# Kernel optimization log

Measured on AMD Instinct MI355X. Metric: run time of the kernel, lower is better.

The kernel has to match this reference:

```python
import jax, jax.numpy as jnp
import numpy as np
import math

B, S = 2, 2048
DIM_MODEL = 2048
NUM_Q_HEADS = 16
GROUP_SIZE = 4
NUM_KV_HEADS = NUM_Q_HEADS // GROUP_SIZE
DIM_K = 128
RMS_EPS = 1e-6
ROPE_BASE = 10000.0


def setup_inputs() -> dict:
    key = jax.random.key(0)
    ks = jax.random.split(key, 8)
    x = jax.random.normal(ks[0], (B, S, DIM_MODEL), dtype=jnp.float32)
    mask = jnp.tril(jnp.ones((S, S), dtype=bool))  # causal
    # Linear weights stored as [in, out] so y = x @ W (bias=False everywhere)
    sd = 1.0 / math.sqrt(DIM_MODEL)
    Wq = jax.random.uniform(ks[1], (DIM_MODEL, DIM_K * NUM_Q_HEADS), jnp.float32, -sd, sd)
    Wk = jax.random.uniform(ks[2], (DIM_MODEL, DIM_K * NUM_KV_HEADS), jnp.float32, -sd, sd)
    Wv = jax.random.uniform(ks[3], (DIM_MODEL, DIM_K * NUM_KV_HEADS), jnp.float32, -sd, sd)
    sf = 1.0 / math.sqrt(DIM_K * NUM_Q_HEADS)
    Wfc = jax.random.uniform(ks[4], (DIM_K * NUM_Q_HEADS, DIM_MODEL), jnp.float32, -sf, sf)
    q_gamma = jnp.ones((DIM_K,), dtype=jnp.float32)
    k_gamma = jnp.ones((DIM_K,), dtype=jnp.float32)
    return {"x": x, "mask": mask, "Wq": Wq, "Wk": Wk, "Wv": Wv,
            "Wfc": Wfc, "q_gamma": q_gamma, "k_gamma": k_gamma}


def _rope(t):
    # t: [B, H, S, D], rotate-half RoPE
    d = t.shape[-1]
    half = d // 2
    inv_freq = 1.0 / (ROPE_BASE ** (jnp.arange(half, dtype=jnp.float32) / half))
    pos = jnp.arange(t.shape[2], dtype=jnp.float32)
    ang = pos[:, None] * inv_freq[None, :]            # [S, half]
    cos, sin = jnp.cos(ang), jnp.sin(ang)              # [S, half]
    t1, t2 = t[..., :half], t[..., half:]
    return jnp.concatenate([t1 * cos - t2 * sin, t2 * cos + t1 * sin], axis=-1)


def _rmsnorm(t, gamma):
    ms = jnp.mean(t * t, axis=-1, keepdims=True)
    return t * jax.lax.rsqrt(ms + RMS_EPS) * gamma


def reference(x, mask, Wq, Wk, Wv, Wfc, q_gamma, k_gamma):
    b, s, _ = x.shape
    q = (x @ Wq).reshape(b, s, NUM_Q_HEADS, DIM_K).transpose(0, 2, 1, 3)   # [B,Hq,S,D]
    k = (x @ Wk).reshape(b, s, NUM_KV_HEADS, DIM_K).transpose(0, 2, 1, 3)  # [B,Hkv,S,D]
    v = (x @ Wv).reshape(b, s, NUM_KV_HEADS, DIM_K).transpose(0, 2, 1, 3)
    q = _rmsnorm(_rope(q), q_gamma)
    k = _rmsnorm(_rope(k), k_gamma)
    q = q.reshape(b, NUM_KV_HEADS, GROUP_SIZE, s, DIM_K)                    # [B,Hkv,G,S,D]
    scores = jnp.einsum('bhgqd,bhkd->bhgqk', q, k) / math.sqrt(DIM_K)      # [B,Hkv,G,S,S]
    scores = jnp.where(mask, scores, -jnp.inf)
    attn = jax.nn.softmax(scores, axis=-1)  # dropout is identity in eval
    out = jnp.einsum('bhgqk,bhkd->bhgqd', attn, v)                          # [B,Hkv,G,S,D]
    out = out.reshape(b, NUM_Q_HEADS, s, DIM_K).transpose(0, 2, 1, 3)
    out = out.reshape(b, s, NUM_Q_HEADS * DIM_K) @ Wfc                      # [B,S,DM]
    return out
```

## Files before the change

kernel.cpp:

```cpp
#include <hip/hip_runtime.h>
#include <hip/hip_bf16.h>

typedef __attribute__((ext_vector_type(8))) short bf16x8;
typedef __attribute__((ext_vector_type(4))) short bf16x4;
typedef __attribute__((ext_vector_type(4))) float f32x4;

#define S_LEN 2048
#define DMODEL 2048
#define NQH 16
#define NKVH 4
#define DK 128

__device__ __forceinline__ float b2f(short u) {
  union { unsigned int i; float f; } x;
  x.i = ((unsigned int)(unsigned short)u) << 16;
  return x.f;
}
__device__ __forceinline__ short f2b(float f) {
  union { float f; unsigned int i; } x; x.f = f;
  unsigned int r = (x.i + 0x7fffu + ((x.i >> 16) & 1u)) >> 16;
  return (short)r;
}
__device__ __forceinline__ unsigned int cvtpk(float a, float b) {
  unsigned int r;
  asm("v_cvt_pk_bf16_f32 %0, %1, %2" : "=v"(r) : "v"(a), "v"(b));
  return r;
}
__device__ __forceinline__ f32x4 mfma16(bf16x8 a, bf16x8 b, f32x4 c) {
  return __builtin_amdgcn_mfma_f32_16x16x32_bf16(a, b, c, 0, 0, 0);
}
__device__ __forceinline__ void async16(short* lds, const short* g) {
  __builtin_amdgcn_global_load_lds(
      (const __attribute__((address_space(1))) unsigned int*)(const void*)g,
      (__attribute__((address_space(3))) unsigned int*)(void*)lds, 16, 0, 0);
}

__global__ void f32_to_bf16(const float* __restrict__ in, short* __restrict__ out, int n4) {
  int i = blockIdx.x * blockDim.x + threadIdx.x;
  if (i >= n4) return;
  float4 v = ((const float4*)in)[i];
  bf16x4 o;
  o[0] = f2b(v.x); o[1] = f2b(v.y); o[2] = f2b(v.z); o[3] = f2b(v.w);
  ((bf16x4*)out)[i] = o;
}

__device__ __forceinline__ void transpose_tile(const float* __restrict__ in,
                                               short* __restrict__ out, int R, int C,
                                               int bx, int by, int tid, short (*t)[33]) {
  const int c0 = bx * 32, r0 = by * 32;
  const int tx = tid & 31, ty = tid >> 5;
#pragma unroll
  for (int i = 0; i < 32; i += 8)
    t[ty + i][tx] = f2b(in[(size_t)(r0 + ty + i) * C + c0 + tx]);
  __syncthreads();
#pragma unroll
  for (int i = 0; i < 32; i += 8)
    out[(size_t)(c0 + ty + i) * R + r0 + tx] = t[tx][ty + i];
}

__global__ __launch_bounds__(256) void prep_kernel(const float* __restrict__ Wq,
                                                   const float* __restrict__ Wk,
                                                   const float* __restrict__ Wv,
                                                   const float* __restrict__ Wfc,
                                                   short* __restrict__ WqT,
                                                   short* __restrict__ WkT,
                                                   short* __restrict__ WvT,
                                                   short* __restrict__ WfcT,
                                                   float* __restrict__ rt) {
  __shared__ short t[32][33];
  const int id = blockIdx.x;
  const int tid = threadIdx.x;
  if (id < 4096) {
    transpose_tile(Wq, WqT, 2048, 2048, id & 63, id >> 6, tid, t);
  } else if (id < 5120) {
    const int r = id - 4096;
    transpose_tile(Wk, WkT, 2048, 512, r & 15, r >> 4, tid, t);
  } else if (id < 6144) {
    const int r = id - 5120;
    transpose_tile(Wv, WvT, 2048, 512, r & 15, r >> 4, tid, t);
  } else if (id < 10240) {
    const int r = id - 6144;
    transpose_tile(Wfc, WfcT, 2048, 2048, r & 63, r >> 6, tid, t);
  } else {
    const int i = (id - 10240) * 256 + tid;
    const int s = i >> 6, d = i & 63;
    float ang = (float)s * __expf((float)d * -0.14391157f);
    float c, sn;
    __sincosf(ang, &sn, &c);
    rt[s * 128 + d] = c;
    rt[s * 128 + 64 + d] = sn;
  }
}

__device__ __forceinline__ void stage_tile64(short* Ls, const short* Gb, int ldg,
                                             int w, int lane) {
#pragma unroll
  for (int i = 0; i < 4; ++i) {
    const int r0 = w * 32 + i * 8;
    const int row = r0 + (lane >> 3);
    const int colb = ((lane & 7) * 8) ^ ((row & 7) << 3);
    async16(Ls + r0 * 64, Gb + (size_t)row * ldg + colb);
  }
}

__global__ __launch_bounds__(256) void gemm_qkv(const short* __restrict__ A,
                                                const short* __restrict__ WT,
                                                short* __restrict__ Qr,
                                                short* __restrict__ Kr,
                                                short* __restrict__ Vtr,
                                                const float* __restrict__ qg,
                                                const float* __restrict__ kg,
                                                const float* __restrict__ ropeT) {
  constexpr int CS_LD = 136;
  __shared__ __align__(16) short smem[4 * 128 * 64];

  const int flat = blockIdx.x;
  const int xcd = flat & 7, idx = flat >> 3;
  const int mb = (xcd >> 1) * 8 + (idx & 7);
  const int nb = (xcd & 1) * 12 + (idx >> 3);

  const int tid = threadIdx.x;
  const int lane = tid & 63;
  const int w = tid >> 6;
  const int wm = w >> 1, wn = w & 1;
  const int l15 = lane & 15, lg = lane >> 4;
  const int K = DMODEL;
  constexpr int NSTEP = DMODEL / 64;

  f32x4 acc[4][4] = {};
  const short* Ab = A + (size_t)mb * 128 * K;
  const short* Bb = WT + (size_t)nb * 128 * K;

  stage_tile64(smem, Ab, K, w, lane);
  stage_tile64(smem + 8192, Bb, K, w, lane);
  asm volatile("s_waitcnt vmcnt(0)" ::: "memory");
  __syncthreads();

  for (int t = 0; t < NSTEP; ++t) {
    const int cur = t & 1;
    short* Ac = smem + cur * 16384;
    short* Bc = Ac + 8192;
    if (t + 1 < NSTEP) {
      short* An = smem + (cur ^ 1) * 16384;
      stage_tile64(An, Ab + (t + 1) * 64, K, w, lane);
      stage_tile64(An + 8192, Bb + (t + 1) * 64, K, w, lane);
    }
#pragma unroll
    for (int kk = 0; kk < 2; ++kk) {
      bf16x8 af[4], bfr[4];
#pragma unroll
      for (int mt = 0; mt < 4; ++mt)
        af[mt] = *(const bf16x8*)(Ac + (wm * 64 + mt * 16 + l15) * 64 +
                                  ((kk * 32 + lg * 8) ^ ((l15 & 7) << 3)));
#pragma unroll
      for (int nt = 0; nt < 4; ++nt)
        bfr[nt] = *(const bf16x8*)(Bc + (wn * 64 + nt * 16 + l15) * 64 +
                                   ((kk * 32 + lg * 8) ^ ((l15 & 7) << 3)));
#pragma unroll
      for (int mt = 0; mt < 4; ++mt)
#pragma unroll
        for (int nt = 0; nt < 4; ++nt)
          acc[mt][nt] = mfma16(af[mt], bfr[nt], acc[mt][nt]);
    }
    asm volatile("s_waitcnt vmcnt(0)" ::: "memory");
    __syncthreads();
  }

  short* Cs = smem;
#pragma unroll
  for (int mt = 0; mt < 4; ++mt)
#pragma unroll
    for (int nt = 0; nt < 4; ++nt)
#pragma unroll
      for (int r = 0; r < 4; ++r)
        Cs[(wm * 64 + mt * 16 + lg * 4 + r) * CS_LD + wn * 64 + nt * 16 + l15] =
            f2b(acc[mt][nt][r]);
  __syncthreads();

  const int srow0 = mb * 128;
  const int b = srow0 >> 11;

  if (nb < 20) {
    const bool isQ = nb < 16;
    const int h = isQ ? nb : nb - 16;
    const float* gamma = isQ ? qg : kg;
    const int r = tid >> 1, half = tid & 1;
    const int s = (srow0 + r) & 2047;
    const float* rt = ropeT + (size_t)s * 128;
    float ss = 0.f;
    bf16x8 ov[8];
#pragma unroll
    for (int j = 0; j < 8; ++j) {
      bf16x8 t1v = *(const bf16x8*)(Cs + r * CS_LD + j * 8);
      bf16x8 t2v = *(const bf16x8*)(Cs + r * CS_LD + 64 + j * 8);
      float4 c0 = *(const float4*)(rt + j * 8);
      float4 c1 = *(const float4*)(rt + j * 8 + 4);
      float4 s0 = *(const float4*)(rt + 64 + j * 8);
      float4 s1 = *(const float4*)(rt + 64 + j * 8 + 4);
      float cc[8] = {c0.x, c0.y, c0.z, c0.w, c1.x, c1.y, c1.z, c1.w};
      float sn[8] = {s0.x, s0.y, s0.z, s0.w, s1.x, s1.y, s1.z, s1.w};
#pragma unroll
      for (int i = 0; i < 8; ++i) {
        float t1 = b2f(t1v[i]), t2 = b2f(t2v[i]);
        float o = half ? (t2 * cc[i] + t1 * sn[i]) : (t1 * cc[i] - t2 * sn[i]);
        ss += o * o;
        ov[j][i] = f2b(o);
      }
    }
    ss += __shfl_xor(ss, 1);
    float inv = rsqrtf(ss * (1.0f / 128.0f) + 1e-6f);
    if (isQ) inv *= (0.08838834764831845f * 1.4426950408889634f);
    const int NH = isQ ? NQH : NKVH;
    short* outp = isQ ? Qr : Kr;
    short* ob = outp + ((size_t)(b * NH + h) * S_LEN + s) * DK + half * 64;
#pragma unroll
    for (int j = 0; j < 8; ++j) {
      float4 g0 = *(const float4*)(gamma + half * 64 + j * 8);
      float4 g1 = *(const float4*)(gamma + half * 64 + j * 8 + 4);
      float gg[8] = {g0.x, g0.y, g0.z, g0.w, g1.x, g1.y, g1.z, g1.w};
      bf16x8 vv;
#pragma unroll
      for (int i = 0; i < 8; ++i) vv[i] = f2b(b2f(ov[j][i]) * inv * gg[i]);
      *(bf16x8*)(ob + j * 8) = vv;
    }
  } else {
    const int h = nb - 20;
    const int d = tid & 127;
    const int sh = tid >> 7;
    const int sbase = (srow0 & 2047) + sh * 64;
    short* ob = Vtr + ((size_t)(b * NKVH + h) * DK + d) * S_LEN + sbase;
    for (int i0 = 0; i0 < 64; i0 += 8) {
      bf16x8 v;
#pragma unroll
      for (int j = 0; j < 8; ++j) {
        const int p = i0 + j;
        const int sl = sh * 64 + 16 * (p & 3) + (p >> 2);
        v[j] = Cs[sl * CS_LD + d];
      }
      *(bf16x8*)(ob + i0) = v;
    }
  }
}

__global__ __launch_bounds__(256) void gemm_out(const short* __restrict__ A,
                                                const short* __restrict__ BT,
                                                float* __restrict__ outf) {
  __shared__ __align__(16) short smem[4 * 128 * 64];

  const int flat = blockIdx.x;
  const int xcd = flat & 7, idx = flat >> 3;
  const int mb = (xcd >> 1) * 8 + (idx & 7);
  const int nb = (xcd & 1) * 8 + (idx >> 3);

  const int tid = threadIdx.x;
  const int lane = tid & 63;
  const int w = tid >> 6;
  const int wm = w >> 1, wn = w & 1;
  const int l15 = lane & 15, lg = lane >> 4;
  const int K = NQH * DK, N = DMODEL;
  constexpr int NSTEP = (NQH * DK) / 64;

  f32x4 acc[4][4] = {};
  const short* Ab = A + (size_t)mb * 128 * K;
  const short* Bb = BT + (size_t)nb * 128 * K;

  stage_tile64(smem, Ab, K, w, lane);
  stage_tile64(smem + 8192, Bb, K, w, lane);
  asm volatile("s_waitcnt vmcnt(0)" ::: "memory");
  __syncthreads();

  for (int t = 0; t < NSTEP; ++t) {
    const int cur = t & 1;
    short* Ac = smem + cur * 16384;
    short* Bc = Ac + 8192;
    if (t + 1 < NSTEP) {
      short* An = smem + (cur ^ 1) * 16384;
      stage_tile64(An, Ab + (t + 1) * 64, K, w, lane);
      stage_tile64(An + 8192, Bb + (t + 1) * 64, K, w, lane);
    }
#pragma unroll
    for (int kk = 0; kk < 2; ++kk) {
      bf16x8 af[4], bfr[4];
#pragma unroll
      for (int mt = 0; mt < 4; ++mt)
        af[mt] = *(const bf16x8*)(Ac + (wm * 64 + mt * 16 + l15) * 64 +
                                  ((kk * 32 + lg * 8) ^ ((l15 & 7) << 3)));
#pragma unroll
      for (int nt = 0; nt < 4; ++nt)
        bfr[nt] = *(const bf16x8*)(Bc + (wn * 64 + nt * 16 + l15) * 64 +
                                   ((kk * 32 + lg * 8) ^ ((l15 & 7) << 3)));
#pragma unroll
      for (int mt = 0; mt < 4; ++mt)
#pragma unroll
        for (int nt = 0; nt < 4; ++nt)
          acc[mt][nt] = mfma16(af[mt], bfr[nt], acc[mt][nt]);
    }
    asm volatile("s_waitcnt vmcnt(0)" ::: "memory");
    __syncthreads();
  }

#pragma unroll
  for (int mt = 0; mt < 4; ++mt) {
    const int row = mb * 128 + wm * 64 + mt * 16 + lg * 4;
#pragma unroll
    for (int nt = 0; nt < 4; ++nt) {
      const int col = nb * 128 + wn * 64 + nt * 16 + l15;
#pragma unroll
      for (int r = 0; r < 4; ++r)
        outf[(size_t)(row + r) * N + col] = acc[mt][nt][r];
    }
  }
}

__device__ __forceinline__ void stage_kv(const short* __restrict__ Kb,
                                         const short* __restrict__ Vb, int kb,
                                         short* Ks, short* Vs, int w, int lane) {
#pragma unroll
  for (int i = 0; i < 4; ++i) {
    const int c = 4 * w + i;
    const int krow = c * 4 + (lane >> 4);
    const int kcol = (((lane & 15) * 16) ^ ((krow & 7) << 4)) >> 1;
    async16(Ks + c * 512, Kb + (size_t)(kb + krow) * DK + kcol);
    const int vrow = c * 8 + (lane >> 3);
    const int vcol = (((lane & 7) * 16) ^ ((vrow & 7) << 4)) >> 1;
    async16(Vs + c * 512, Vb + (size_t)vrow * S_LEN + kb + vcol);
  }
}

__device__ __forceinline__ void sm_pv(f32x4* sc, float* lsum, f32x4* acco,
                                      const short* Vc, short* Pw, int q0, bool diag,
                                      int kb, int l15, int lg) {
  if (diag) {
#pragma unroll
    for (int nt = 0; nt < 4; ++nt) {
      const int k = kb + nt * 16 + l15;
#pragma unroll
      for (int r = 0; r < 4; ++r)
        if (k > q0 + lg * 4 + r) sc[nt][r] = -1e30f;
    }
  }
#pragma unroll
  for (int r = 0; r < 4; ++r) {
    const float p0 = exp2f(sc[0][r]);
    const float p1 = exp2f(sc[1][r]);
    const float p2 = exp2f(sc[2][r]);
    const float p3 = exp2f(sc[3][r]);
    lsum[r] += (p0 + p1) + (p2 + p3);
    uint2 dv;
    dv.x = cvtpk(p0, p1);
    dv.y = cvtpk(p2, p3);
    *(uint2*)(Pw + (lg * 4 + r) * 72 + l15 * 4) = dv;
  }
#pragma unroll
  for (int kk = 0; kk < 2; ++kk) {
    bf16x8 ap = *(const bf16x8*)(Pw + l15 * 72 + kk * 32 + lg * 8);
#pragma unroll
    for (int dt = 0; dt < 8; ++dt) {
      const int vrow = dt * 16 + l15;
      bf16x8 bv = *(const bf16x8*)(Vc + vrow * 64 +
                                   (((kk * 64 + lg * 16) ^ ((vrow & 7) << 4)) >> 1));
      acco[dt] = mfma16(ap, bv, acco[dt]);
    }
  }
}

__device__ __forceinline__ void attn_writeout(f32x4* acco, float* lsum,
                                              short* __restrict__ AO, int b, int qh,
                                              int q0, int l15, int lg) {
  float ls[4];
#pragma unroll
  for (int r = 0; r < 4; ++r) {
    float t = lsum[r];
    t += __shfl_xor(t, 1);
    t += __shfl_xor(t, 2);
    t += __shfl_xor(t, 4);
    t += __shfl_xor(t, 8);
    ls[r] = 1.0f / t;
  }
  short* ob = AO + (size_t)(b * S_LEN + q0) * (NQH * DK) + qh * DK;
#pragma unroll
  for (int dt = 0; dt < 8; ++dt)
#pragma unroll
    for (int r = 0; r < 4; ++r)
      ob[(size_t)(lg * 4 + r) * (NQH * DK) + dt * 16 + l15] = f2b(acco[dt][r] * ls[r]);
}

__global__ __launch_bounds__(256, 2) void attn_kernel(const short* __restrict__ Qr,
                                                      const short* __restrict__ Kr,
                                                      const short* __restrict__ Vt,
                                                      short* __restrict__ AO) {
  const int flat = blockIdx.x;
  const int nw = (flat & 7) * 64 + (flat >> 3);
  const int qtA = nw & 15;
  const int bh = nw >> 4;
  const int qtB = 31 - qtA;
  const int b = bh >> 4, qh = bh & 15;
  const int kvh = qh >> 2;
  const short* Qb = Qr + (size_t)bh * S_LEN * DK;
  const short* Kb = Kr + (size_t)(b * NKVH + kvh) * S_LEN * DK;
  const short* Vb = Vt + (size_t)(b * NKVH + kvh) * DK * S_LEN;
  const int tid = threadIdx.x, lane = tid & 63, w = tid >> 6;
  const int l15 = lane & 15, lg = lane >> 4;

  __shared__ __align__(16) short KV[4][64 * 128];
  __shared__ __align__(16) short P[4][16][72];
  short* Pw = &P[w][0][0];

  const int q0A = qtA * 64 + w * 16, q0B = qtB * 64 + w * 16;
  bf16x8 aqA[4], aqB[4];
#pragma unroll
  for (int kk = 0; kk < 4; ++kk) {
    aqA[kk] = *(const bf16x8*)(Qb + (size_t)(q0A + l15) * DK + kk * 32 + lg * 8);
    aqB[kk] = *(const bf16x8*)(Qb + (size_t)(q0B + l15) * DK + kk * 32 + lg * 8);
  }

  f32x4 accoA[8] = {}, accoB[8] = {};
  float lsA[4] = {0.f, 0.f, 0.f, 0.f}, lsB[4] = {0.f, 0.f, 0.f, 0.f};

  short* Kcur = KV[0]; short* Vcur = KV[1];
  short* Knxt = KV[2]; short* Vnxt = KV[3];

  stage_kv(Kb, Vb, 0, Kcur, Vcur, w, lane);
  asm volatile("s_waitcnt vmcnt(0)" ::: "memory");
  __syncthreads();

  for (int kt = 0; kt <= qtB; ++kt) {
    const int kb = kt * 64;
    if (kt < qtB) stage_kv(Kb, Vb, kb + 64, Knxt, Vnxt, w, lane);

    if (kt <= qtA) {
      f32x4 scB[4] = {}, scA[4] = {};
#pragma unroll
      for (int kk = 0; kk < 4; ++kk)
#pragma unroll
        for (int nt = 0; nt < 4; ++nt) {
          const int krow = nt * 16 + l15;
          bf16x8 bk = *(const bf16x8*)(Kcur + krow * 128 +
                                       (((kk * 64 + lg * 16) ^ ((krow & 7) << 4)) >> 1));
          scB[nt] = mfma16(aqB[kk], bk, scB[nt]);
          scA[nt] = mfma16(aqA[kk], bk, scA[nt]);
        }
      sm_pv(scB, lsB, accoB, Vcur, Pw, q0B, false, kb, l15, lg);
      sm_pv(scA, lsA, accoA, Vcur, Pw, q0A, kt == qtA, kb, l15, lg);
    } else {
      f32x4 scB[4] = {};
#pragma unroll
      for (int kk = 0; kk < 4; ++kk)
#pragma unroll
        for (int nt = 0; nt < 4; ++nt) {
          const int krow = nt * 16 + l15;
          bf16x8 bk = *(const bf16x8*)(Kcur + krow * 128 +
                                       (((kk * 64 + lg * 16) ^ ((krow & 7) << 4)) >> 1));
          scB[nt] = mfma16(aqB[kk], bk, scB[nt]);
        }
      sm_pv(scB, lsB, accoB, Vcur, Pw, q0B, kt == qtB, kb, l15, lg);
    }

    asm volatile("s_waitcnt vmcnt(0)" ::: "memory");
    __syncthreads();
    short* t;
    t = Kcur; Kcur = Knxt; Knxt = t;
    t = Vcur; Vcur = Vnxt; Vnxt = t;
  }

  attn_writeout(accoB, lsB, AO, b, qh, q0B, l15, lg);
  attn_writeout(accoA, lsA, AO, b, qh, q0A, l15, lg);
}

extern "C" void kernel_launch(void* const* d_in, const int* in_sizes, int n_in,
                              void* d_out, int out_size, void* d_ws, size_t ws_size,
                              hipStream_t stream) {
  const float* x = (const float*)d_in[0];
  const float* Wq = (const float*)d_in[2];
  const float* Wk = (const float*)d_in[3];
  const float* Wv = (const float*)d_in[4];
  const float* Wfc = (const float*)d_in[5];
  const float* qg = (const float*)d_in[6];
  const float* kg = (const float*)d_in[7];

  short* ws = (short*)d_ws;
  short* xb = ws;
  short* WqkvT = xb + (size_t)4096 * 2048;
  short* WqT = WqkvT;
  short* WkT = WqT + (size_t)2048 * 2048;
  short* WvT = WkT + (size_t)512 * 2048;
  short* WfcT = WvT + (size_t)512 * 2048;
  short* Qr = WfcT + (size_t)2048 * 2048;
  short* Kr = Qr + (size_t)32 * 2048 * 128;
  short* Vt = Kr + (size_t)8 * 2048 * 128;
  float* ropeT = (float*)(Vt + (size_t)8 * 128 * 2048);
  short* AO = xb;

  f32_to_bf16<<<(4096 * 2048 / 4 + 255) / 256, 256, 0, stream>>>(x, xb, 4096 * 2048 / 4);
  prep_kernel<<<10752, 256, 0, stream>>>(Wq, Wk, Wv, Wfc, WqT, WkT, WvT, WfcT, ropeT);

  gemm_qkv<<<768, 256, 0, stream>>>(xb, WqkvT, Qr, Kr, Vt, qg, kg, ropeT);

  attn_kernel<<<512, 256, 0, stream>>>(Qr, Kr, Vt, AO);

  gemm_out<<<512, 256, 0, stream>>>(AO, WfcT, (float*)d_out);
}
```

Measured before the change: 191.6 us.

## Shrink GEMM K-step to 32 for 4-block occupancy and fold x conversion into prep

The fp32-to-bf16 conversion of x moves into the prep kernel, removing one launch. The two GEMMs share a new core that stages 32-wide K slices with a different XOR swizzle, which cuts LDS from 64KB to 32KB and sets launch_bounds(256,4) so more blocks fit per CU. The QKV epilogue now processes the 128-row tile in two 64-row phases to fit the smaller LDS, with four threads per row for RoPE and RMSNorm. The cost is twice as many barriers per K and more serialized epilogue phases.

```diff
diff --git a/kernel.cpp b/kernel.cpp
--- a/kernel.cpp
+++ b/kernel.cpp
@@ -35,15 +35,6 @@
       (__attribute__((address_space(3))) unsigned int*)(void*)lds, 16, 0, 0);
 }
 
-__global__ void f32_to_bf16(const float* __restrict__ in, short* __restrict__ out, int n4) {
-  int i = blockIdx.x * blockDim.x + threadIdx.x;
-  if (i >= n4) return;
-  float4 v = ((const float4*)in)[i];
-  bf16x4 o;
-  o[0] = f2b(v.x); o[1] = f2b(v.y); o[2] = f2b(v.z); o[3] = f2b(v.w);
-  ((bf16x4*)out)[i] = o;
-}
-
 __device__ __forceinline__ void transpose_tile(const float* __restrict__ in,
                                                short* __restrict__ out, int R, int C,
                                                int bx, int by, int tid, short (*t)[33]) {
@@ -58,10 +49,12 @@
     out[(size_t)(c0 + ty + i) * R + r0 + tx] = t[tx][ty + i];
 }
 
-__global__ __launch_bounds__(256) void prep_kernel(const float* __restrict__ Wq,
+__global__ __launch_bounds__(256) void prep_kernel(const float* __restrict__ x,
+                                                   const float* __restrict__ Wq,
                                                    const float* __restrict__ Wk,
                                                    const float* __restrict__ Wv,
                                                    const float* __restrict__ Wfc,
+                                                   short* __restrict__ xb,
                                                    short* __restrict__ WqT,
                                                    short* __restrict__ WkT,
                                                    short* __restrict__ WvT,
@@ -70,19 +63,26 @@
   __shared__ short t[32][33];
   const int id = blockIdx.x;
   const int tid = threadIdx.x;
-  if (id < 4096) {
-    transpose_tile(Wq, WqT, 2048, 2048, id & 63, id >> 6, tid, t);
-  } else if (id < 5120) {
-    const int r = id - 4096;
+  if (id < 8192) {
+    const int i = id * 256 + tid;
+    float4 v = ((const float4*)x)[i];
+    bf16x4 o;
+    o[0] = f2b(v.x); o[1] = f2b(v.y); o[2] = f2b(v.z); o[3] = f2b(v.w);
+    ((bf16x4*)xb)[i] = o;
+  } else if (id < 12288) {
+    const int r = id - 8192;
+    transpose_tile(Wq, WqT, 2048, 2048, r & 63, r >> 6, tid, t);
+  } else if (id < 13312) {
+    const int r = id - 12288;
     transpose_tile(Wk, WkT, 2048, 512, r & 15, r >> 4, tid, t);
-  } else if (id < 6144) {
-    const int r = id - 5120;
+  } else if (id < 14336) {
+    const int r = id - 13312;
     transpose_tile(Wv, WvT, 2048, 512, r & 15, r >> 4, tid, t);
-  } else if (id < 10240) {
-    const int r = id - 6144;
+  } else if (id < 18432) {
+    const int r = id - 14336;
     transpose_tile(Wfc, WfcT, 2048, 2048, r & 63, r >> 6, tid, t);
   } else {
-    const int i = (id - 10240) * 256 + tid;
+    const int i = (id - 18432) * 256 + tid;
     const int s = i >> 6, d = i & 63;
     float ang = (float)s * __expf((float)d * -0.14391157f);
     float c, sn;
@@ -92,27 +92,81 @@
   }
 }
 
-__device__ __forceinline__ void stage_tile64(short* Ls, const short* Gb, int ldg,
-                                             int w, int lane) {
-#pragma unroll
-  for (int i = 0; i < 4; ++i) {
-    const int r0 = w * 32 + i * 8;
-    const int row = r0 + (lane >> 3);
-    const int colb = ((lane & 7) * 8) ^ ((row & 7) << 3);
-    async16(Ls + r0 * 64, Gb + (size_t)row * ldg + colb);
-  }
-}
-
-__global__ __launch_bounds__(256) void gemm_qkv(const short* __restrict__ A,
-                                                const short* __restrict__ WT,
-                                                short* __restrict__ Qr,
-                                                short* __restrict__ Kr,
-                                                short* __restrict__ Vtr,
-                                                const float* __restrict__ qg,
-                                                const float* __restrict__ kg,
-                                                const float* __restrict__ ropeT) {
-  constexpr int CS_LD = 136;
-  __shared__ __align__(16) short smem[4 * 128 * 64];
+__device__ __forceinline__ void gemm128_core(const short* __restrict__ Ab,
+                                             const short* __restrict__ Bb,
+                                             short* sm, f32x4 (&acc)[4][4],
+                                             int tid, int K) {
+  const int lane = tid & 63, w = tid >> 6;
+  const int wm = w >> 1, wn = w & 1;
+  const int l15 = lane & 15, lg = lane >> 4;
+  constexpr int ABUF = 4096;
+  constexpr int BUFSZ = 8192;
+
+  const int sr = lane >> 2, sc = lane & 3;
+  const int r0 = w * 32 + sr, r1 = r0 + 16;
+  const short* gA0 = Ab + (size_t)r0 * K + ((sc ^ ((r0 >> 1) & 3)) * 8);
+  const short* gA1 = Ab + (size_t)r1 * K + ((sc ^ ((r1 >> 1) & 3)) * 8);
+  const short* gB0 = Bb + (size_t)r0 * K + ((sc ^ ((r0 >> 1) & 3)) * 8);
+  const short* gB1 = Bb + (size_t)r1 * K + ((sc ^ ((r1 >> 1) & 3)) * 8);
+  const int dA0 = w * 1024, dA1 = dA0 + 512;
+  const int dB0 = ABUF + dA0, dB1 = ABUF + dA1;
+
+  int aoff[4], boff[4];
+#pragma unroll
+  for (int mt = 0; mt < 4; ++mt) {
+    const int row = wm * 64 + mt * 16 + l15;
+    aoff[mt] = row * 32 + ((lg * 8) ^ (((row >> 1) & 3) * 8));
+  }
+#pragma unroll
+  for (int nt = 0; nt < 4; ++nt) {
+    const int row = wn * 64 + nt * 16 + l15;
+    boff[nt] = ABUF + row * 32 + ((lg * 8) ^ (((row >> 1) & 3) * 8));
+  }
+
+  auto stage = [&](int buf, int t) {
+    short* d = sm + buf * BUFSZ;
+    const int o = t * 32;
+    async16(d + dA0, gA0 + o);
+    async16(d + dA1, gA1 + o);
+    async16(d + dB0, gB0 + o);
+    async16(d + dB1, gB1 + o);
+  };
+
+  const int NSTEP = K / 32;
+  stage(0, 0);
+  asm volatile("s_waitcnt vmcnt(0)" ::: "memory");
+  __syncthreads();
+
+#pragma unroll 1
+  for (int t = 0; t < NSTEP; ++t) {
+    const int cur = t & 1;
+    const short* bc = sm + cur * BUFSZ;
+    if (t + 1 < NSTEP) stage(cur ^ 1, t + 1);
+    bf16x8 af[4], bfr[4];
+#pragma unroll
+    for (int mt = 0; mt < 4; ++mt) af[mt] = *(const bf16x8*)(bc + aoff[mt]);
+#pragma unroll
+    for (int nt = 0; nt < 4; ++nt) bfr[nt] = *(const bf16x8*)(bc + boff[nt]);
+#pragma unroll
+    for (int mt = 0; mt < 4; ++mt)
+#pragma unroll
+      for (int nt = 0; nt < 4; ++nt)
+        acc[mt][nt] = mfma16(af[mt], bfr[nt], acc[mt][nt]);
+    asm volatile("s_waitcnt vmcnt(0)" ::: "memory");
+    __syncthreads();
+  }
+}
+
+__global__ __launch_bounds__(256, 4) void gemm_qkv(const short* __restrict__ A,
+                                                   const short* __restrict__ WT,
+                                                   short* __restrict__ Qr,
+                                                   short* __restrict__ Kr,
+                                                   short* __restrict__ Vtr,
+                                                   const float* __restrict__ qg,
+                                                   const float* __restrict__ kg,
+                                                   const float* __restrict__ ropeT) {
+  constexpr int CL = 136;
+  __shared__ __align__(16) short smem[16384];
 
   const int flat = blockIdx.x;
   const int xcd = flat & 7, idx = flat >> 3;
@@ -120,132 +174,105 @@
   const int nb = (xcd & 1) * 12 + (idx >> 3);
 
   const int tid = threadIdx.x;
-  const int lane = tid & 63;
-  const int w = tid >> 6;
+  const int lane = tid & 63, w = tid >> 6;
   const int wm = w >> 1, wn = w & 1;
   const int l15 = lane & 15, lg = lane >> 4;
-  const int K = DMODEL;
-  constexpr int NSTEP = DMODEL / 64;
 
   f32x4 acc[4][4] = {};
-  const short* Ab = A + (size_t)mb * 128 * K;
-  const short* Bb = WT + (size_t)nb * 128 * K;
-
-  stage_tile64(smem, Ab, K, w, lane);
-  stage_tile64(smem + 8192, Bb, K, w, lane);
-  asm volatile("s_waitcnt vmcnt(0)" ::: "memory");
-  __syncthreads();
-
-  for (int t = 0; t < NSTEP; ++t) {
-    const int cur = t & 1;
-    short* Ac = smem + cur * 16384;
-    short* Bc = Ac + 8192;
-    if (t + 1 < NSTEP) {
-      short* An = smem + (cur ^ 1) * 16384;
-      stage_tile64(An, Ab + (t + 1) * 64, K, w, lane);
-      stage_tile64(An + 8192, Bb + (t + 1) * 64, K, w, lane);
-    }
-#pragma unroll
-    for (int kk = 0; kk < 2; ++kk) {
-      bf16x8 af[4], bfr[4];
-#pragma unroll
-      for (int mt = 0; mt < 4; ++mt)
-        af[mt] = *(const bf16x8*)(Ac + (wm * 64 + mt * 16 + l15) * 64 +
-                                  ((kk * 32 + lg * 8) ^ ((l15 & 7) << 3)));
-#pragma unroll
-      for (int nt = 0; nt < 4; ++nt)
-        bfr[nt] = *(const bf16x8*)(Bc + (wn * 64 + nt * 16 + l15) * 64 +
-                                   ((kk * 32 + lg * 8) ^ ((l15 & 7) << 3)));
-#pragma unroll
-      for (int mt = 0; mt < 4; ++mt)
-#pragma unroll
-        for (int nt = 0; nt < 4; ++nt)
-          acc[mt][nt] = mfma16(af[mt], bfr[nt], acc[mt][nt]);
-    }
-    asm volatile("s_waitcnt vmcnt(0)" ::: "memory");
-    __syncthreads();
-  }
-
-  short* Cs = smem;
-#pragma unroll
-  for (int mt = 0; mt < 4; ++mt)
-#pragma unroll
-    for (int nt = 0; nt < 4; ++nt)
-#pragma unroll
-      for (int r = 0; r < 4; ++r)
-        Cs[(wm * 64 + mt * 16 + lg * 4 + r) * CS_LD + wn * 64 + nt * 16 + l15] =
-            f2b(acc[mt][nt][r]);
-  __syncthreads();
+  gemm128_core(A + (size_t)mb * 128 * DMODEL, WT + (size_t)nb * 128 * DMODEL,
+               smem, acc, tid, DMODEL);
 
   const int srow0 = mb * 128;
   const int b = srow0 >> 11;
-
-  if (nb < 20) {
-    const bool isQ = nb < 16;
-    const int h = isQ ? nb : nb - 16;
-    const float* gamma = isQ ? qg : kg;
-    const int r = tid >> 1, half = tid & 1;
-    const int s = (srow0 + r) & 2047;
-    const float* rt = ropeT + (size_t)s * 128;
-    float ss = 0.f;
-    bf16x8 ov[8];
-#pragma unroll
-    for (int j = 0; j < 8; ++j) {
-      bf16x8 t1v = *(const bf16x8*)(Cs + r * CS_LD + j * 8);
-      bf16x8 t2v = *(const bf16x8*)(Cs + r * CS_LD + 64 + j * 8);
-      float4 c0 = *(const float4*)(rt + j * 8);
-      float4 c1 = *(const float4*)(rt + j * 8 + 4);
-      float4 s0 = *(const float4*)(rt + 64 + j * 8);
-      float4 s1 = *(const float4*)(rt + 64 + j * 8 + 4);
-      float cc[8] = {c0.x, c0.y, c0.z, c0.w, c1.x, c1.y, c1.z, c1.w};
-      float sn[8] = {s0.x, s0.y, s0.z, s0.w, s1.x, s1.y, s1.z, s1.w};
-#pragma unroll
-      for (int i = 0; i < 8; ++i) {
-        float t1 = b2f(t1v[i]), t2 = b2f(t2v[i]);
-        float o = half ? (t2 * cc[i] + t1 * sn[i]) : (t1 * cc[i] - t2 * sn[i]);
-        ss += o * o;
-        ov[j][i] = f2b(o);
+  short* Cs = smem;
+
+  for (int ph = 0; ph < 2; ++ph) {
+    __syncthreads();
+    if (wm == ph) {
+#pragma unroll
+      for (int mt = 0; mt < 4; ++mt)
+#pragma unroll
+        for (int nt = 0; nt < 4; ++nt)
+#pragma unroll
+          for (int rr = 0; rr < 4; ++rr)
+            Cs[(mt * 16 + lg * 4 + rr) * CL + wn * 64 + nt * 16 + l15] =
+                f2b(acc[mt][nt][rr]);
+    }
+    __syncthreads();
+
+    if (nb < 20) {
+      const bool isQ = nb < 16;
+      const int h = isQ ? nb : nb - 16;
+      const float* gamma = isQ ? qg : kg;
+      const int r = tid >> 2, quad = tid & 3;
+      const int half = quad & 1, qd = quad >> 1;
+      const int s = (srow0 + ph * 64 + r) & 2047;
+      const float* rt = ropeT + (size_t)s * 128;
+      const short* crow = Cs + r * CL;
+      float ss = 0.f;
+      bf16x8 ov[4];
+#pragma unroll
+      for (int j = 0; j < 4; ++j) {
+        const int d = qd * 32 + j * 8;
+        bf16x8 t1v = *(const bf16x8*)(crow + d);
+        bf16x8 t2v = *(const bf16x8*)(crow + 64 + d);
+        float4 c0 = *(const float4*)(rt + d);
+        float4 c1 = *(const float4*)(rt + d + 4);
+        float4 s0 = *(const float4*)(rt + 64 + d);
+        float4 s1 = *(const float4*)(rt + 64 + d + 4);
+        float cc[8] = {c0.x, c0.y, c0.z, c0.w, c1.x, c1.y, c1.z, c1.w};
+        float sn[8] = {s0.x, s0.y, s0.z, s0.w, s1.x, s1.y, s1.z, s1.w};
+#pragma unroll
+        for (int i = 0; i < 8; ++i) {
+          float t1 = b2f(t1v[i]), t2 = b2f(t2v[i]);
+          float o = half ? (t2 * cc[i] + t1 * sn[i]) : (t1 * cc[i] - t2 * sn[i]);
+          ss += o * o;
+          ov[j][i] = f2b(o);
+        }
       }
-    }
-    ss += __shfl_xor(ss, 1);
-    float inv = rsqrtf(ss * (1.0f / 128.0f) + 1e-6f);
-    if (isQ) inv *= (0.08838834764831845f * 1.4426950408889634f);
-    const int NH = isQ ? NQH : NKVH;
-    short* outp = isQ ? Qr : Kr;
-    short* ob = outp + ((size_t)(b * NH + h) * S_LEN + s) * DK + half * 64;
-#pragma unroll
-    for (int j = 0; j < 8; ++j) {
-      float4 g0 = *(const float4*)(gamma + half * 64 + j * 8);
-      float4 g1 = *(const float4*)(gamma + half * 64 + j * 8 + 4);
-      float gg[8] = {g0.x, g0.y, g0.z, g0.w, g1.x, g1.y, g1.z, g1.w};
-      bf16x8 vv;
-#pragma unroll
-      for (int i = 0; i < 8; ++i) vv[i] = f2b(b2f(ov[j][i]) * inv * gg[i]);
-      *(bf16x8*)(ob + j * 8) = vv;
-    }
-  } else {
-    const int h = nb - 20;
-    const int d = tid & 127;
-    const int sh = tid >> 7;
-    const int sbase = (srow0 & 2047) + sh * 64;
-    short* ob = Vtr + ((size_t)(b * NKVH + h) * DK + d) * S_LEN + sbase;
-    for (int i0 = 0; i0 < 64; i0 += 8) {
-      bf16x8 v;
-#pragma unroll
-      for (int j = 0; j < 8; ++j) {
-        const int p = i0 + j;
-        const int sl = sh * 64 + 16 * (p & 3) + (p >> 2);
-        v[j] = Cs[sl * CS_LD + d];
+      ss += __shfl_xor(ss, 1);
+      ss += __shfl_xor(ss, 2);
+      float inv = rsqrtf(ss * (1.0f / 128.0f) + 1e-6f);
+      if (isQ) inv *= (0.08838834764831845f * 1.4426950408889634f);
+      const int NH = isQ ? NQH : NKVH;
+      short* outp = isQ ? Qr : Kr;
+      short* ob = outp + ((size_t)(b * NH + h) * S_LEN + s) * DK + half * 64 + qd * 32;
+#pragma unroll
+      for (int j = 0; j < 4; ++j) {
+        const int d = qd * 32 + j * 8;
+        float4 g0 = *(const float4*)(gamma + half * 64 + d);
+        float4 g1 = *(const float4*)(gamma + half * 64 + d + 4);
+        float gg[8] = {g0.x, g0.y, g0.z, g0.w, g1.x, g1.y, g1.z, g1.w};
+        bf16x8 vv;
+#pragma unroll
+        for (int i = 0; i < 8; ++i) vv[i] = f2b(b2f(ov[j][i]) * inv * gg[i]);
+        *(bf16x8*)(ob + j * 8) = vv;
       }
-      *(bf16x8*)(ob + i0) = v;
-    }
-  }
-}
-
-__global__ __launch_bounds__(256) void gemm_out(const short* __restrict__ A,
-                                                const short* __restrict__ BT,
-                                                float* __restrict__ outf) {
-  __shared__ __align__(16) short smem[4 * 128 * 64];
+    } else {
+      const int h = nb - 20;
+      const int d = tid & 127;
+      const int hi = tid >> 7;
+      const int sbase = ((srow0 + ph * 64) & 2047);
+      short* ob = Vtr + ((size_t)(b * NKVH + h) * DK + d) * S_LEN + sbase;
+      const short* cc = Cs + d;
+      for (int i0 = hi * 32; i0 < hi * 32 + 32; i0 += 8) {
+        bf16x8 v;
+#pragma unroll
+        for (int j = 0; j < 8; ++j) {
+          const int p = i0 + j;
+          const int sl = 16 * (p & 3) + (p >> 2);
+          v[j] = cc[sl * CL];
+        }
+        *(bf16x8*)(ob + i0) = v;
+      }
+    }
+  }
+}
+
+__global__ __launch_bounds__(256, 4) void gemm_out(const short* __restrict__ A,
+                                                   const short* __restrict__ BT,
+                                                   float* __restrict__ outf) {
+  __shared__ __align__(16) short smem[16384];
 
   const int flat = blockIdx.x;
   const int xcd = flat & 7, idx = flat >> 3;
@@ -253,51 +280,14 @@
   const int nb = (xcd & 1) * 8 + (idx >> 3);
 
   const int tid = threadIdx.x;
-  const int lane = tid & 63;
-  const int w = tid >> 6;
+  const int lane = tid & 63, w = tid >> 6;
   const int wm = w >> 1, wn = w & 1;
   const int l15 = lane & 15, lg = lane >> 4;
-  const int K = NQH * DK, N = DMODEL;
-  constexpr int NSTEP = (NQH * DK) / 64;
+  const int K = NQH * DK;
 
   f32x4 acc[4][4] = {};
-  const short* Ab = A + (size_t)mb * 128 * K;
-  const short* Bb = BT + (size_t)nb * 128 * K;
-
-  stage_tile64(smem, Ab, K, w, lane);
-  stage_tile64(smem + 8192, Bb, K, w, lane);
-  asm volatile("s_waitcnt vmcnt(0)" ::: "memory");
-  __syncthreads();
-
-  for (int t = 0; t < NSTEP; ++t) {
-    const int cur = t & 1;
-    short* Ac = smem + cur * 16384;
-    short* Bc = Ac + 8192;
-    if (t + 1 < NSTEP) {
-      short* An = smem + (cur ^ 1) * 16384;
-      stage_tile64(An, Ab + (t + 1) * 64, K, w, lane);
-      stage_tile64(An + 8192, Bb + (t + 1) * 64, K, w, lane);
-    }
-#pragma unroll
-    for (int kk = 0; kk < 2; ++kk) {
-      bf16x8 af[4], bfr[4];
-#pragma unroll
-      for (int mt = 0; mt < 4; ++mt)
-        af[mt] = *(const bf16x8*)(Ac + (wm * 64 + mt * 16 + l15) * 64 +
-                                  ((kk * 32 + lg * 8) ^ ((l15 & 7) << 3)));
-#pragma unroll
-      for (int nt = 0; nt < 4; ++nt)
-        bfr[nt] = *(const bf16x8*)(Bc + (wn * 64 + nt * 16 + l15) * 64 +
-                                   ((kk * 32 + lg * 8) ^ ((l15 & 7) << 3)));
-#pragma unroll
-      for (int mt = 0; mt < 4; ++mt)
-#pragma unroll
-        for (int nt = 0; nt < 4; ++nt)
-          acc[mt][nt] = mfma16(af[mt], bfr[nt], acc[mt][nt]);
-    }
-    asm volatile("s_waitcnt vmcnt(0)" ::: "memory");
-    __syncthreads();
-  }
+  gemm128_core(A + (size_t)mb * 128 * K, BT + (size_t)nb * 128 * K,
+               smem, acc, tid, K);
 
 #pragma unroll
   for (int mt = 0; mt < 4; ++mt) {
@@ -307,7 +297,7 @@
       const int col = nb * 128 + wn * 64 + nt * 16 + l15;
 #pragma unroll
       for (int r = 0; r < 4; ++r)
-        outf[(size_t)(row + r) * N + col] = acc[mt][nt][r];
+        outf[(size_t)(row + r) * DMODEL + col] = acc[mt][nt][r];
     }
   }
 }
@@ -491,8 +481,8 @@
   float* ropeT = (float*)(Vt + (size_t)8 * 128 * 2048);
   short* AO = xb;
 
-  f32_to_bf16<<<(4096 * 2048 / 4 + 255) / 256, 256, 0, stream>>>(x, xb, 4096 * 2048 / 4);
-  prep_kernel<<<10752, 256, 0, stream>>>(Wq, Wk, Wv, Wfc, WqT, WkT, WvT, WfcT, ropeT);
+  prep_kernel<<<18944, 256, 0, stream>>>(x, Wq, Wk, Wv, Wfc, xb, WqT, WkT, WvT,
+                                         WfcT, ropeT);
 
   gemm_qkv<<<768, 256, 0, stream>>>(xb, WqkvT, Qr, Kr, Vt, qg, kg, ropeT);
 
```

Result: slower. 208.2 us (+8.7%).
